# Kernel tuning notes

Hardware: AMD Instinct MI355X
Metric: run time of the kernel (lower is better)

## Reference

```python
import jax, jax.numpy as jnp
import numpy as np

N_EMBED = 384
HEAD_SIZE = 64
B, T = 512, 256


def setup_inputs() -> dict:
    key = jax.random.key(0)
    kx, kq, kk, kv = jax.random.split(key, 4)
    x = jax.random.normal(kx, (B, T, N_EMBED), dtype=jnp.float32)
    # nn.Linear(n_embed, head_size, bias=False): y = x @ W^T with W [head_size, n_embed].
    # We store the transposed [n_embed, head_size] matrices directly.
    s = 1.0 / np.sqrt(N_EMBED)
    Wq = jax.random.uniform(kq, (N_EMBED, HEAD_SIZE), jnp.float32, -s, s)
    Wk = jax.random.uniform(kk, (N_EMBED, HEAD_SIZE), jnp.float32, -s, s)
    Wv = jax.random.uniform(kv, (N_EMBED, HEAD_SIZE), jnp.float32, -s, s)
    return {"x": x, "Wq": Wq, "Wk": Wk, "Wv": Wv}


def reference(x, Wq, Wk, Wv):
    # Single-head causal self-attention (dropout in eval mode = identity).
    q = jnp.einsum("btc,cd->btd", x, Wq)  # [B,T,D]
    k = jnp.einsum("btc,cd->btd", x, Wk)
    v = jnp.einsum("btc,cd->btd", x, Wv)
    scale = jnp.asarray(k.shape[-1], x.dtype) ** -0.5
    wei = jnp.einsum("btd,bsd->bts", q, k) * scale  # [B,T,T]
    t = wei.shape[-1]
    causal = jnp.tril(jnp.ones((t, t), dtype=bool))
    wei = jnp.where(causal, wei, -jnp.inf)
    wei = jax.nn.softmax(wei, axis=-1)
    out = jnp.einsum("bts,bsd->btd", wei, v)  # [B,T,D]
    return out
```

## Files before the change

### kernel.cpp

```cpp
#include <hip/hip_runtime.h>

#define BATCH 512
#define SEQ   256
#define CEMB  384
#define HD    64
#define MROWS (BATCH*SEQ)

typedef __bf16 bf16_t;
typedef __bf16 bf16x4 __attribute__((ext_vector_type(4)));
typedef __bf16 bf16x8 __attribute__((ext_vector_type(8)));
typedef float  f32x4  __attribute__((ext_vector_type(4)));

#define GLOAD_LDS16(gp, lp) \
    __builtin_amdgcn_global_load_lds((const __attribute__((address_space(1))) void*)(gp), \
                                     (__attribute__((address_space(3))) void*)(lp), 16, 0, 0)

__global__ void wconv_kernel(const float* __restrict__ Wq, const float* __restrict__ Wk,
                             const float* __restrict__ Wv, bf16_t* __restrict__ Wf) {
    int idx = blockIdx.x * 256 + threadIdx.x;
    if (idx >= 144 * 512) return;
    int j = idx & 7, lane = (idx >> 3) & 63, f = idx >> 9;
    int ni = f % 12, s = f / 12;
    int n = ni * 16 + (lane & 15);
    int k = s * 32 + ((lane >> 4) << 3) + j;
    const float* W = (n < 64) ? Wq : ((n < 128) ? Wk : Wv);
    Wf[idx] = (bf16_t)W[k * HD + (n & 63)];
}

__device__ inline bf16x8 cvt8(float4 a, float4 b) {
    bf16x8 r;
    r[0] = (bf16_t)a.x; r[1] = (bf16_t)a.y; r[2] = (bf16_t)a.z; r[3] = (bf16_t)a.w;
    r[4] = (bf16_t)b.x; r[5] = (bf16_t)b.y; r[6] = (bf16_t)b.z; r[7] = (bf16_t)b.w;
    return r;
}

__global__ __launch_bounds__(768, 3)
void qkv_kernel(const float* __restrict__ x, const bf16_t* __restrict__ Wf,
                bf16_t* __restrict__ qg, bf16_t* __restrict__ kg, bf16_t* __restrict__ vg) {
    __shared__ char smem[147456];

    const int tid = threadIdx.x;
    const int w = tid >> 6, lane = tid & 63;
    const int l15 = lane & 15, l4 = lane >> 4;

    #pragma unroll
    for (int i = 0; i < 12; ++i)
        GLOAD_LDS16((const char*)Wf + tid * 16 + i * 12288, smem + tid * 16 + i * 12288);
    __syncthreads();

    const char* wp = smem + lane * 16;
    const long rowbase = (long)blockIdx.x * 192 + w * 16;
    const long arow = rowbase + l15;
    const long arowc = (arow < MROWS) ? arow : (MROWS - 1);
    const float* aptr = x + arowc * CEMB + l4 * 8;

    f32x4 acc[12];
    #pragma unroll
    for (int ni = 0; ni < 12; ++ni) acc[ni] = f32x4{0.f, 0.f, 0.f, 0.f};

    #pragma unroll
    for (int hf = 0; hf < 2; ++hf) {
        float4 A[6][2];
        #pragma unroll
        for (int s = 0; s < 6; ++s) {
            A[s][0] = *(const float4*)(aptr + (hf * 6 + s) * 32);
            A[s][1] = *(const float4*)(aptr + (hf * 6 + s) * 32 + 4);
        }
        #pragma unroll
        for (int s = 0; s < 6; ++s) {
            bf16x8 af = cvt8(A[s][0], A[s][1]);
            const int ks = hf * 6 + s;
            #pragma unroll
            for (int ni = 0; ni < 12; ++ni) {
                bf16x8 bf = *(const bf16x8*)(wp + (ks * 12 + ni) * 1024);
                acc[ni] = __builtin_amdgcn_mfma_f32_16x16x32_bf16(af, bf, acc[ni], 0, 0, 0);
            }
        }
    }

    if (rowbase < MROWS) {
        #pragma unroll
        for (int ni = 0; ni < 12; ++ni) {
            int col = ni * 16 + l15;
            bf16_t* dst = (col < 64) ? qg : ((col < 128) ? kg : vg);
            int d = col & 63;
            #pragma unroll
            for (int r = 0; r < 4; ++r) {
                long rg = rowbase + l4 * 4 + r;
                dst[rg * HD + d] = (bf16_t)acc[ni][r];
            }
        }
    }
}

__global__ __launch_bounds__(256, 2)
void attn_kernel(const bf16_t* __restrict__ qg, const bf16_t* __restrict__ kg,
                 const bf16_t* __restrict__ vg, float* __restrict__ out) {
    __shared__ char smem[81920];

    const int tid = threadIdx.x;
    const int w = tid >> 6, lane = tid & 63;
    const int l15 = lane & 15, l4 = lane >> 4;
    const long base = (long)blockIdx.x * SEQ * HD;

    for (int it = 0; it < 8; ++it) {
        int i = tid + it * 256;
        int s = i >> 3, cb = (i & 7) * 16;
        bf16x8 kv = *(const bf16x8*)(kg + base + (long)i * 8);
        *(bf16x8*)(smem + s * 128 + (cb ^ ((s & 7) << 4))) = kv;
    }
    for (int it = 0; it < 8; ++it) {
        int i = tid + it * 256;
        int s = i >> 3, d0 = (i & 7) * 8;
        bf16x8 vv = *(const bf16x8*)(vg + base + (long)i * 8);
        #pragma unroll
        for (int j = 0; j < 8; ++j) {
            int d = d0 + j;
            *(bf16_t*)(smem + 32768 + d * 512 + ((s * 2) ^ ((d & 7) << 4))) = vv[j];
        }
    }

    bf16x8 qf[4][2];
    #pragma unroll
    for (int mi = 0; mi < 4; ++mi) {
        int row = mi * 64 + w * 16 + l15;
        #pragma unroll
        for (int kk = 0; kk < 2; ++kk)
            qf[mi][kk] = *(const bf16x8*)(qg + base + (long)row * HD + kk * 32 + l4 * 8);
    }

    __syncthreads();

    f32x4 oacc[4][4];
    float mrow[4][4], lrow[4][4];
    #pragma unroll
    for (int mi = 0; mi < 4; ++mi) {
        #pragma unroll
        for (int di = 0; di < 4; ++di) oacc[mi][di] = f32x4{0.f, 0.f, 0.f, 0.f};
        #pragma unroll
        for (int r = 0; r < 4; ++r) { mrow[mi][r] = -1e30f; lrow[mi][r] = 0.f; }
    }

    char* Pw = smem + 65536 + w * 4096;
    const int ntiles = (w < 2) ? 7 : 8;
    const float LOG2E = 1.44269504089f;

    for (int st = 0; st < ntiles; ++st) {
        f32x4 sacc[4][2];
        #pragma unroll
        for (int mi = 0; mi < 4; ++mi)
            #pragma unroll
            for (int ni = 0; ni < 2; ++ni) sacc[mi][ni] = f32x4{0.f, 0.f, 0.f, 0.f};

        #pragma unroll
        for (int kk = 0; kk < 2; ++kk) {
            #pragma unroll
            for (int ni = 0; ni < 2; ++ni) {
                int s = st * 32 + ni * 16 + l15;
                bf16x8 kf = *(const bf16x8*)(smem + s * 128 + (((kk * 32 + l4 * 8) * 2) ^ ((s & 7) << 4)));
                #pragma unroll
                for (int mi = 0; mi < 4; ++mi) {
                    if (st * 32 <= mi * 64 + w * 16 + 15)
                        sacc[mi][ni] = __builtin_amdgcn_mfma_f32_16x16x32_bf16(qf[mi][kk], kf, sacc[mi][ni], 0, 0, 0);
                }
            }
        }

        #pragma unroll
        for (int mi = 0; mi < 4; ++mi) {
            const int R = mi * 64 + w * 16;
            if (st * 32 > R + 15) continue;
            const bool needmask = (st * 32 + 31 > R);
            #pragma unroll
            for (int r = 0; r < 4; ++r) {
                float s0 = sacc[mi][0][r] * 0.125f;
                float s1 = sacc[mi][1][r] * 0.125f;
                if (needmask) {
                    int row = R + l4 * 4 + r;
                    if (st * 32 + l15 > row)      s0 = -1e30f;
                    if (st * 32 + 16 + l15 > row) s1 = -1e30f;
                }
                float mx = fmaxf(s0, s1);
                mx = fmaxf(mx, __shfl_xor(mx, 1));
                mx = fmaxf(mx, __shfl_xor(mx, 2));
                mx = fmaxf(mx, __shfl_xor(mx, 4));
                mx = fmaxf(mx, __shfl_xor(mx, 8));
                float mold = mrow[mi][r];
                float mnew = fmaxf(mold, mx);
                float alpha = exp2f((mold - mnew) * LOG2E);
                float p0 = exp2f((s0 - mnew) * LOG2E);
                float p1 = exp2f((s1 - mnew) * LOG2E);
                mrow[mi][r] = mnew;
                float rs = p0 + p1;
                rs += __shfl_xor(rs, 1);
                rs += __shfl_xor(rs, 2);
                rs += __shfl_xor(rs, 4);
                rs += __shfl_xor(rs, 8);
                lrow[mi][r] = lrow[mi][r] * alpha + rs;
                #pragma unroll
                for (int di = 0; di < 4; ++di) oacc[mi][di][r] *= alpha;
                int q = mi * 16 + l4 * 4 + r;
                *(bf16_t*)(Pw + q * 64 + ((l15 * 2) ^ ((q & 3) << 4))) = (bf16_t)p0;
                *(bf16_t*)(Pw + q * 64 + ((32 + l15 * 2) ^ ((q & 3) << 4))) = (bf16_t)p1;
            }
        }

        #pragma unroll
        for (int mi = 0; mi < 4; ++mi) {
            if (st * 32 > mi * 64 + w * 16 + 15) continue;
            int q = mi * 16 + l15;
            bf16x8 pf = *(const bf16x8*)(Pw + q * 64 + ((l4 * 16) ^ ((q & 3) << 4)));
            #pragma unroll
            for (int di = 0; di < 4; ++di) {
                int d = di * 16 + l15;
                bf16x8 vf = *(const bf16x8*)(smem + 32768 + d * 512 + (((st * 32 + l4 * 8) * 2) ^ ((d & 7) << 4)));
                oacc[mi][di] = __builtin_amdgcn_mfma_f32_16x16x32_bf16(pf, vf, oacc[mi][di], 0, 0, 0);
            }
        }
    }

    #pragma unroll
    for (int mi = 0; mi < 4; ++mi) {
        #pragma unroll
        for (int r = 0; r < 4; ++r) {
            float inv = 1.f / lrow[mi][r];
            long row = mi * 64 + w * 16 + l4 * 4 + r;
            #pragma unroll
            for (int di = 0; di < 4; ++di)
                out[base + row * HD + di * 16 + l15] = oacc[mi][di][r] * inv;
        }
    }
}

extern "C" void kernel_launch(void* const* d_in, const int* in_sizes, int n_in,
                              void* d_out, int out_size, void* d_ws, size_t ws_size,
                              hipStream_t stream) {
    const float* x  = (const float*)d_in[0];
    const float* Wq = (const float*)d_in[1];
    const float* Wk = (const float*)d_in[2];
    const float* Wv = (const float*)d_in[3];
    float* out = (float*)d_out;

    bf16_t* Wf = (bf16_t*)d_ws;
    bf16_t* qg = (bf16_t*)((char*)d_ws + (1 << 20));
    bf16_t* kg = qg + (long)MROWS * HD;
    bf16_t* vg = kg + (long)MROWS * HD;

    wconv_kernel<<<dim3(288), dim3(256), 0, stream>>>(Wq, Wk, Wv, Wf);
    qkv_kernel<<<dim3((MROWS + 191) / 192), dim3(768), 0, stream>>>(x, Wf, qg, kg, vg);
    attn_kernel<<<dim3(BATCH), dim3(256), 0, stream>>>(qg, kg, vg, out);
}
```

Baseline: 98.86 us.

## Retile QKV GEMM warps to 64 rows x 48 columns for LDS reuse

Each of the 12 warps in the QKV projection now computes a 64-row by 48-column output tile (4 row fragments x 3 column fragments) instead of a 16-row by 192-column strip. This cuts LDS weight reads per MFMA from one per MFMA to three per twelve, at the cost of each warp loading four rows of x from global memory. Each x row is now loaded redundantly by four warps (through cache) instead of once.

```diff
diff --git a/kernel.cpp b/kernel.cpp
--- a/kernel.cpp
+++ b/kernel.cpp
@@ -49,45 +49,57 @@
     __syncthreads();
 
     const char* wp = smem + lane * 16;
-    const long rowbase = (long)blockIdx.x * 192 + w * 16;
-    const long arow = rowbase + l15;
-    const long arowc = (arow < MROWS) ? arow : (MROWS - 1);
-    const float* aptr = x + arowc * CEMB + l4 * 8;
-
-    f32x4 acc[12];
-    #pragma unroll
-    for (int ni = 0; ni < 12; ++ni) acc[ni] = f32x4{0.f, 0.f, 0.f, 0.f};
-
-    #pragma unroll
-    for (int hf = 0; hf < 2; ++hf) {
-        float4 A[6][2];
-        #pragma unroll
-        for (int s = 0; s < 6; ++s) {
-            A[s][0] = *(const float4*)(aptr + (hf * 6 + s) * 32);
-            A[s][1] = *(const float4*)(aptr + (hf * 6 + s) * 32 + 4);
-        }
-        #pragma unroll
-        for (int s = 0; s < 6; ++s) {
-            bf16x8 af = cvt8(A[s][0], A[s][1]);
-            const int ks = hf * 6 + s;
-            #pragma unroll
-            for (int ni = 0; ni < 12; ++ni) {
-                bf16x8 bf = *(const bf16x8*)(wp + (ks * 12 + ni) * 1024);
-                acc[ni] = __builtin_amdgcn_mfma_f32_16x16x32_bf16(af, bf, acc[ni], 0, 0, 0);
-            }
-        }
-    }
-
-    if (rowbase < MROWS) {
-        #pragma unroll
-        for (int ni = 0; ni < 12; ++ni) {
-            int col = ni * 16 + l15;
+    const int ni0 = (w & 3) * 3;
+    const long rowbase = (long)blockIdx.x * 192 + (w >> 2) * 64;
+
+    const float* aptr[4];
+    #pragma unroll
+    for (int fr = 0; fr < 4; ++fr) {
+        long arow = rowbase + fr * 16 + l15;
+        long arowc = (arow < MROWS) ? arow : (MROWS - 1);
+        aptr[fr] = x + arowc * CEMB + l4 * 8;
+    }
+
+    f32x4 acc[4][3];
+    #pragma unroll
+    for (int fr = 0; fr < 4; ++fr)
+        #pragma unroll
+        for (int nj = 0; nj < 3; ++nj) acc[fr][nj] = f32x4{0.f, 0.f, 0.f, 0.f};
+
+    #pragma unroll
+    for (int ks = 0; ks < 12; ++ks) {
+        float4 Araw[4][2];
+        #pragma unroll
+        for (int fr = 0; fr < 4; ++fr) {
+            Araw[fr][0] = *(const float4*)(aptr[fr] + ks * 32);
+            Araw[fr][1] = *(const float4*)(aptr[fr] + ks * 32 + 4);
+        }
+        bf16x8 B[3];
+        #pragma unroll
+        for (int nj = 0; nj < 3; ++nj)
+            B[nj] = *(const bf16x8*)(wp + (ks * 12 + ni0 + nj) * 1024);
+        bf16x8 af[4];
+        #pragma unroll
+        for (int fr = 0; fr < 4; ++fr) af[fr] = cvt8(Araw[fr][0], Araw[fr][1]);
+        #pragma unroll
+        for (int fr = 0; fr < 4; ++fr)
+            #pragma unroll
+            for (int nj = 0; nj < 3; ++nj)
+                acc[fr][nj] = __builtin_amdgcn_mfma_f32_16x16x32_bf16(af[fr], B[nj], acc[fr][nj], 0, 0, 0);
+    }
+
+    #pragma unroll
+    for (int fr = 0; fr < 4; ++fr) {
+        if (rowbase + fr * 16 >= MROWS) continue;
+        #pragma unroll
+        for (int nj = 0; nj < 3; ++nj) {
+            int col = (ni0 + nj) * 16 + l15;
             bf16_t* dst = (col < 64) ? qg : ((col < 128) ? kg : vg);
             int d = col & 63;
             #pragma unroll
             for (int r = 0; r < 4; ++r) {
-                long rg = rowbase + l4 * 4 + r;
-                dst[rg * HD + d] = (bf16_t)acc[ni][r];
+                long rg = rowbase + fr * 16 + l4 * 4 + r;
+                dst[rg * HD + d] = (bf16_t)acc[fr][nj][r];
             }
         }
     }
```

Measured after the change: 157.1 us. 58.9% more time.
